# Optimization experiments

Hardware: AMD Instinct MI355X
Metric: run time of the kernel (lower is better)

Reference implementation:

```python
import jax, jax.numpy as jnp
import numpy as np

DIM = 1024
CTX_DIM = 1024
VALUE_DIM = 1024
HEADS = 16
HEAD_DIM = DIM // HEADS        # q/k head dim = 64
V_HEAD_DIM = VALUE_DIM // HEADS
LN_EPS = 1e-5


def setup_inputs() -> dict:
    key = jax.random.key(0)
    k0, k1, k2, k3, k4 = jax.random.split(key, 5)
    B, N, M = 4, 1024, 1024
    x = jax.random.normal(k0, (B, N, DIM), jnp.float32)
    context = jax.random.normal(k1, (B, M, CTX_DIM), jnp.float32)
    # Linear weights stored as [in, out] (y = x @ W), matching torch Linear math
    Wq = jax.random.normal(k2, (DIM, DIM), jnp.float32) * (DIM ** -0.5)
    Wkv = jax.random.normal(k3, (CTX_DIM, DIM + VALUE_DIM), jnp.float32) * (CTX_DIM ** -0.5)
    Wt = jax.random.normal(k4, (HEADS, HEADS), jnp.float32) * (HEADS ** -0.5)
    gamma = jnp.ones((HEADS,), jnp.float32)
    beta = jnp.zeros((HEADS,), jnp.float32)
    return {"x": x, "context": context, "Wq": Wq, "Wkv": Wkv,
            "Wt": Wt, "gamma": gamma, "beta": beta}


def reference(x, context, Wq, Wkv, Wt, gamma, beta):
    B, N, _ = x.shape
    M = context.shape[1]
    # projections
    q = (x @ Wq).reshape(B, N, HEADS, HEAD_DIM).transpose(0, 2, 1, 3)       # [B,H,N,d]
    kv = context @ Wkv                                                      # [B,M,dim+vdim]
    k = kv[..., :DIM].reshape(B, M, HEADS, HEAD_DIM).transpose(0, 2, 1, 3)  # [B,H,M,d]
    v = kv[..., DIM:].reshape(B, M, HEADS, V_HEAD_DIM).transpose(0, 2, 1, 3)
    # scaled dot-product scores, fully materialized as in the original
    scale = HEAD_DIM ** -0.5
    dots = jnp.einsum('bhid,bhjd->bhij', q * scale, k)                      # [B,H,N,M]
    w = jax.nn.softmax(dots, axis=-1)
    # talking heads: Linear(heads,heads,bias=False) then LayerNorm(heads) over head axis
    w = jnp.einsum('bhij,hg->bgij', w, Wt)
    mu = jnp.mean(w, axis=1, keepdims=True)
    var = jnp.var(w, axis=1, keepdims=True)
    w = (w - mu) * jax.lax.rsqrt(var + LN_EPS)
    w = w * gamma[None, :, None, None] + beta[None, :, None, None]
    attn = jnp.einsum('bhij,bhjd->bhid', w, v)                              # [B,H,N,vd]
    out = attn.transpose(0, 2, 1, 3).reshape(B, N, VALUE_DIM)
    return out
```

## Files before the change

### kernel.cpp

```cpp
#include <hip/hip_runtime.h>
#include <hip/hip_bf16.h>

typedef __bf16 bf16;
typedef bf16 bf16x2 __attribute__((ext_vector_type(2)));
typedef bf16 bf16x4 __attribute__((ext_vector_type(4)));
typedef bf16 bf16x8 __attribute__((ext_vector_type(8)));
typedef float floatx4 __attribute__((ext_vector_type(4)));

#define MFMA_BF16(a, b, c) __builtin_amdgcn_mfma_f32_16x16x32_bf16((a), (b), (c), 0, 0, 0)

__global__ __launch_bounds__(256) void cvt_kernel(const float* __restrict__ in,
                                                  bf16* __restrict__ out, int n8) {
    int idx = blockIdx.x * 256 + threadIdx.x;
    if (idx >= n8) return;
    const float* src = in + (size_t)idx * 8;
    float4 f0 = *(const float4*)src;
    float4 f1 = *(const float4*)(src + 4);
    bf16x8 v = {(bf16)f0.x, (bf16)f0.y, (bf16)f0.z, (bf16)f0.w,
                (bf16)f1.x, (bf16)f1.y, (bf16)f1.z, (bf16)f1.w};
    *(bf16x8*)(out + (size_t)idx * 8) = v;
}

__global__ __launch_bounds__(256) void trans_kernel(const float* __restrict__ in,
                                                    bf16* __restrict__ out, int R, int C) {
    __shared__ float tile[32][33];
    const int t = threadIdx.x;
    const int r0 = blockIdx.y * 32, c0 = blockIdx.x * 32;
    int r = t >> 3, c4 = (t & 7) * 4;
    float4 v = *(const float4*)&in[(size_t)(r0 + r) * C + c0 + c4];
    tile[r][c4 + 0] = v.x; tile[r][c4 + 1] = v.y;
    tile[r][c4 + 2] = v.z; tile[r][c4 + 3] = v.w;
    __syncthreads();
    int rp = t >> 3, cp = (t & 7) * 4;
    bf16x4 w = {(bf16)tile[cp + 0][rp], (bf16)tile[cp + 1][rp],
                (bf16)tile[cp + 2][rp], (bf16)tile[cp + 3][rp]};
    *(bf16x4*)&out[(size_t)(c0 + rp) * R + r0 + cp] = w;
}

__global__ __launch_bounds__(256) void vtrans_kernel(const bf16* __restrict__ in,
                                                     bf16* __restrict__ out) {
    __shared__ bf16 tile[32][36];
    const int t = threadIdx.x;
    const int r0 = blockIdx.y * 32, c0 = blockIdx.x * 32;
    int r = t >> 3, c4 = (t & 7) * 4;
    bf16x4 v = *(const bf16x4*)&in[(size_t)(r0 + r) * 1024 + c0 + c4];
    tile[r][c4 + 0] = v[0]; tile[r][c4 + 1] = v[1];
    tile[r][c4 + 2] = v[2]; tile[r][c4 + 3] = v[3];
    __syncthreads();
    int rp = t >> 3, cp = (t & 7) * 4;
    int hd = c0 + rp;
    int b = r0 >> 10, j = (r0 & 1023) + cp;
    bf16x4 w = {tile[cp + 0][rp], tile[cp + 1][rp], tile[cp + 2][rp], tile[cp + 3][rp]};
    *(bf16x4*)&out[(size_t)(b * 1024 + hd) * 1024 + j] = w;
}

__global__ __launch_bounds__(256) void prep_wt_kernel(const float* __restrict__ Wt,
                                                      bf16* __restrict__ WtcT) {
    const int t = threadIdx.x;
    const int g = t >> 4, k = t & 15;
    float s = 0.f;
#pragma unroll
    for (int gg = 0; gg < 16; ++gg) s += Wt[k * 16 + gg];
    WtcT[g * 32 + k] = (bf16)(Wt[k * 16 + g] - s * 0.0625f);
    WtcT[g * 32 + 16 + k] = (bf16)0.f;
}

template <int MODE>
__global__ __launch_bounds__(256) void gemm128(const bf16* __restrict__ A,
                                               const bf16* __restrict__ B,
                                               bf16* __restrict__ C,
                                               bf16* __restrict__ V, int N) {
    __shared__ bf16 As[128 * 40];
    __shared__ bf16 Bs[128 * 40];
    const int t = threadIdx.x;
    const int wv = t >> 6, lane = t & 63, quad = lane >> 4, l15 = lane & 15;
    const int wr = wv >> 1, wc = wv & 1;
    const int m0 = blockIdx.y * 128, n0 = blockIdx.x * 128;
    const int ra = t >> 1, kc = (t & 1) * 16;

    floatx4 acc[4][4] = {};

    for (int k0 = 0; k0 < 1024; k0 += 32) {
        bf16x8 a0 = *(const bf16x8*)&A[(size_t)(m0 + ra) * 1024 + k0 + kc];
        bf16x8 a1 = *(const bf16x8*)&A[(size_t)(m0 + ra) * 1024 + k0 + kc + 8];
        bf16x8 b0 = *(const bf16x8*)&B[(size_t)(n0 + ra) * 1024 + k0 + kc];
        bf16x8 b1 = *(const bf16x8*)&B[(size_t)(n0 + ra) * 1024 + k0 + kc + 8];
        __syncthreads();
        *(bf16x8*)&As[ra * 40 + kc] = a0;
        *(bf16x8*)&As[ra * 40 + kc + 8] = a1;
        *(bf16x8*)&Bs[ra * 40 + kc] = b0;
        *(bf16x8*)&Bs[ra * 40 + kc + 8] = b1;
        __syncthreads();
        bf16x8 af[4], bfr[4];
#pragma unroll
        for (int mt = 0; mt < 4; ++mt)
            af[mt] = *(bf16x8*)&As[(wr * 64 + mt * 16 + l15) * 40 + quad * 8];
#pragma unroll
        for (int nt = 0; nt < 4; ++nt)
            bfr[nt] = *(bf16x8*)&Bs[(wc * 64 + nt * 16 + l15) * 40 + quad * 8];
#pragma unroll
        for (int mt = 0; mt < 4; ++mt)
#pragma unroll
            for (int nt = 0; nt < 4; ++nt)
                acc[mt][nt] = MFMA_BF16(af[mt], bfr[nt], acc[mt][nt]);
    }
#pragma unroll
    for (int mt = 0; mt < 4; ++mt)
#pragma unroll
        for (int nt = 0; nt < 4; ++nt)
#pragma unroll
            for (int r = 0; r < 4; ++r) {
                int m = m0 + wr * 64 + mt * 16 + quad * 4 + r;
                int n = n0 + wc * 64 + nt * 16 + l15;
                bf16 val = (bf16)acc[mt][nt][r];
                if (MODE == 0) {
                    C[(size_t)m * N + n] = val;
                } else {
                    if (n < 1024) C[(size_t)m * 1024 + n] = val;
                    else          V[(size_t)m * 1024 + (n - 1024)] = val;
                }
            }
}

__global__ __launch_bounds__(256, 4) void denom_kernel(const bf16* __restrict__ Qb,
                                                       const bf16* __restrict__ Kb,
                                                       float* __restrict__ L) {
    const int t = threadIdx.x;
    const int wv = t >> 6, lane = t & 63, quad = lane >> 4, l15 = lane & 15;
    unsigned n = blockIdx.x + (blockIdx.y << 5) + (blockIdx.z << 7);
    unsigned o = (n & 7) * 256 + (n >> 3);
    const int i0 = (o & 31) * 32;
    const int b  = (o >> 5) & 3;
    const int jz = o >> 7;
    const float scale = 0.125f;
    const bf16* Kbase = Kb + (size_t)b * 1024 * 1024;

    for (int hh = 0; hh < 4; ++hh) {
        const int h = wv * 4 + hh;
        bf16x8 qa[2][2];
#pragma unroll
        for (int it = 0; it < 2; ++it) {
            const bf16* qp = Qb + (size_t)(b * 1024 + i0 + it * 16 + l15) * 1024 +
                             h * 64 + quad * 8;
            qa[it][0] = *(const bf16x8*)qp;
            qa[it][1] = *(const bf16x8*)(qp + 32);
        }
        floatx4 se[2] = {};
#pragma unroll
        for (int jt = 0; jt < 4; ++jt) {
            int j = jz * 64 + jt * 16 + l15;
            const bf16* kp = Kbase + (size_t)j * 1024 + h * 64 + quad * 8;
            bf16x8 k0 = *(const bf16x8*)kp;
            bf16x8 k1 = *(const bf16x8*)(kp + 32);
#pragma unroll
            for (int it = 0; it < 2; ++it) {
                floatx4 c = {0.f, 0.f, 0.f, 0.f};
                c = MFMA_BF16(qa[it][0], k0, c);
                c = MFMA_BF16(qa[it][1], k1, c);
#pragma unroll
                for (int r = 0; r < 4; ++r) se[it][r] += __expf(c[r] * scale);
            }
        }
#pragma unroll
        for (int it = 0; it < 2; ++it)
#pragma unroll
            for (int r = 0; r < 4; ++r) {
                float s = se[it][r];
                s += __shfl_xor(s, 1); s += __shfl_xor(s, 2);
                s += __shfl_xor(s, 4); s += __shfl_xor(s, 8);
                if (l15 == 0)
                    atomicAdd(&L[(size_t)(b * 16 + h) * 1024 + i0 + it * 16 +
                                 quad * 4 + r], s);
            }
    }
}

__global__ __launch_bounds__(512, 4) void attn_kernel(const bf16* __restrict__ Qb,
                                                      const bf16* __restrict__ Kb,
                                                      const bf16* __restrict__ Vt,
                                                      const float* __restrict__ L,
                                                      const bf16* __restrict__ WtcT,
                                                      const float* __restrict__ gamma,
                                                      const float* __restrict__ beta,
                                                      float* __restrict__ out) {
    __shared__ bf16 Buf1[2][512 * 20];
    __shared__ bf16 Buf2[2][16 * 640];
    const int t = threadIdx.x;
    const int wv = t >> 6, lane = t & 63, quad = lane >> 4, l15 = lane & 15;
    unsigned n = blockIdx.x + (blockIdx.y << 6) + (blockIdx.z << 8);
    unsigned o_idx = (n & 7) * 64 + (n >> 3);
    const int i0 = (o_idx & 63) * 16;
    const int b  = (o_idx >> 6) & 3;
    const int jz = o_idx >> 8;
    const float scale = 0.125f;

    if (t < 8) Buf2[0][2560 + t] = (bf16)0.f;
    const bf16* Zbuf = &Buf2[0][2560];

    bf16x8 a_wt = *(const bf16x8*)&WtcT[l15 * 32 + quad * 8];
    float gq[4], bq[4];
#pragma unroll
    for (int r = 0; r < 4; ++r) { gq[r] = gamma[quad * 4 + r]; bq[r] = beta[quad * 4 + r]; }

    bf16x8 qa[2][2];
    float invl[2][4];
#pragma unroll
    for (int hh = 0; hh < 2; ++hh) {
        int h = wv * 2 + hh;
        const bf16* qp = Qb + (size_t)(b * 1024 + i0 + l15) * 1024 + h * 64 + quad * 8;
        qa[hh][0] = *(const bf16x8*)qp;
        qa[hh][1] = *(const bf16x8*)(qp + 32);
#pragma unroll
        for (int r = 0; r < 4; ++r)
            invl[hh][r] = 1.f / L[(size_t)(b * 16 + h) * 1024 + i0 + quad * 4 + r];
    }

    const bf16* Kbase = Kb + (size_t)b * 1024 * 1024;
    const bf16* Vbase = Vt + (size_t)b * 16 * 64 * 1024;
    floatx4 o[2][4] = {};

    auto S_phase = [&](int jt) {
        bf16* B1 = Buf1[jt & 1];
        const int j0 = jz * 512 + jt * 32;
#pragma unroll
        for (int ns = 0; ns < 2; ++ns) {
            floatx4 cw[2];
#pragma unroll
            for (int hh = 0; hh < 2; ++hh) {
                int h = wv * 2 + hh;
                const bf16* kp = Kbase + (size_t)(j0 + ns * 16 + l15) * 1024 + h * 64 + quad * 8;
                floatx4 c = {0.f, 0.f, 0.f, 0.f};
                c = MFMA_BF16(qa[hh][0], *(const bf16x8*)kp, c);
                c = MFMA_BF16(qa[hh][1], *(const bf16x8*)(kp + 32), c);
                cw[hh] = c;
            }
#pragma unroll
            for (int r = 0; r < 4; ++r) {
                bf16x2 pk = {(bf16)(__expf(cw[0][r] * scale) * invl[0][r]),
                             (bf16)(__expf(cw[1][r] * scale) * invl[1][r])};
                *(bf16x2*)&B1[((quad * 4 + r) * 32 + ns * 16 + l15) * 20 + wv * 2] = pk;
            }
        }
    };
    auto MIX = [&](int jt) {
        const bf16* B1 = Buf1[jt & 1];
        bf16* B2 = Buf2[jt & 1];
#pragma unroll
        for (int grp = 0; grp < 4; ++grp) {
            int gi = wv * 4 + grp, ig = gi >> 1, jb = (gi & 1) * 16;
            int p = ig * 32 + jb + l15;
            const bf16* src = (quad < 2) ? &B1[p * 20 + quad * 8] : Zbuf;
            floatx4 c = {0.f, 0.f, 0.f, 0.f};
            c = MFMA_BF16(a_wt, *(const bf16x8*)src, c);
            float s2 = c[0] * c[0] + c[1] * c[1] + c[2] * c[2] + c[3] * c[3];
            s2 += __shfl_xor(s2, 16);
            s2 += __shfl_xor(s2, 32);
            float rs = rsqrtf(s2 * 0.0625f + 1e-5f);
#pragma unroll
            for (int r = 0; r < 4; ++r) {
                float w2 = c[r] * rs * gq[r] + bq[r];
                B2[(quad * 4 + r) * 640 + (quad & 1) * 8 + ig * 40 + jb + l15] = (bf16)w2;
            }
        }
    };
    auto PV = [&](int jt) {
        const bf16* B2 = Buf2[jt & 1];
        const int j0 = jz * 512 + jt * 32;
#pragma unroll
        for (int hh = 0; hh < 2; ++hh) {
            int g = wv * 2 + hh;
            bf16x8 a = *(const bf16x8*)&B2[g * 640 + ((g >> 2) & 1) * 8 + l15 * 40 + quad * 8];
#pragma unroll
            for (int dt = 0; dt < 4; ++dt) {
                const bf16* vp = Vbase + (size_t)(g * 64 + dt * 16 + l15) * 1024 + j0 + quad * 8;
                o[hh][dt] = MFMA_BF16(a, *(const bf16x8*)vp, o[hh][dt]);
            }
        }
    };

    S_phase(0);
    __syncthreads();
    S_phase(1); MIX(0);
    __syncthreads();
    for (int jt = 2; jt < 16; ++jt) {
        S_phase(jt); PV(jt - 2); MIX(jt - 1);
        __syncthreads();
    }
    PV(14); MIX(15);
    __syncthreads();
    PV(15);

#pragma unroll
    for (int hh = 0; hh < 2; ++hh) {
        int g = wv * 2 + hh;
#pragma unroll
        for (int dt = 0; dt < 4; ++dt)
#pragma unroll
            for (int r = 0; r < 4; ++r)
                atomicAdd(&out[(size_t)(b * 1024 + i0 + quad * 4 + r) * 1024 +
                               g * 64 + dt * 16 + l15], o[hh][dt][r]);
    }
}

extern "C" void kernel_launch(void* const* d_in, const int* in_sizes, int n_in,
                              void* d_out, int out_size, void* d_ws, size_t ws_size,
                              hipStream_t stream) {
    const float* x     = (const float*)d_in[0];
    const float* ctx   = (const float*)d_in[1];
    const float* Wq    = (const float*)d_in[2];
    const float* Wkv   = (const float*)d_in[3];
    const float* Wt    = (const float*)d_in[4];
    const float* gamma = (const float*)d_in[5];
    const float* beta  = (const float*)d_in[6];
    float* out = (float*)d_out;

    bf16* xb   = (bf16*)d_ws;
    bf16* cb   = xb + (size_t)4 * 1024 * 1024;
    bf16* WqT  = cb + (size_t)4 * 1024 * 1024;
    bf16* WkvT = WqT + (size_t)1024 * 1024;
    bf16* Qb   = WkvT + (size_t)2048 * 1024;
    bf16* Kb   = Qb + (size_t)4 * 1024 * 1024;
    bf16* Vr   = Kb + (size_t)4 * 1024 * 1024;
    bf16* Vt   = Vr + (size_t)4 * 1024 * 1024;
    float* L   = (float*)(Vt + (size_t)4 * 1024 * 1024);
    bf16* WtcT = Vr;

    hipMemsetAsync(L, 0, (size_t)4 * 16 * 1024 * sizeof(float), stream);
    hipMemsetAsync(out, 0, (size_t)out_size * sizeof(float), stream);

    cvt_kernel<<<2048, 256, 0, stream>>>(x, xb, 524288);
    cvt_kernel<<<2048, 256, 0, stream>>>(ctx, cb, 524288);
    trans_kernel<<<dim3(32, 32), 256, 0, stream>>>(Wq, WqT, 1024, 1024);
    trans_kernel<<<dim3(64, 32), 256, 0, stream>>>(Wkv, WkvT, 1024, 2048);

    gemm128<0><<<dim3(8, 32), 256, 0, stream>>>(xb, WqT, Qb, nullptr, 1024);
    gemm128<1><<<dim3(16, 32), 256, 0, stream>>>(cb, WkvT, Kb, Vr, 2048);
    vtrans_kernel<<<dim3(32, 128), 256, 0, stream>>>(Vr, Vt);
    prep_wt_kernel<<<1, 256, 0, stream>>>(Wt, WtcT);

    denom_kernel<<<dim3(32, 4, 16), 256, 0, stream>>>(Qb, Kb, L);
    attn_kernel<<<dim3(64, 4, 2), 512, 0, stream>>>(Qb, Kb, Vt, L, WtcT, gamma, beta, out);
}
```

Baseline: 369.5 us.

## Fuse softmax denominator computation into attention kernel, removing denom kernel

```diff
diff --git a/kernel.cpp b/kernel.cpp
--- a/kernel.cpp
+++ b/kernel.cpp
@@ -122,63 +122,9 @@
             }
 }
 
-__global__ __launch_bounds__(256, 4) void denom_kernel(const bf16* __restrict__ Qb,
-                                                       const bf16* __restrict__ Kb,
-                                                       float* __restrict__ L) {
-    const int t = threadIdx.x;
-    const int wv = t >> 6, lane = t & 63, quad = lane >> 4, l15 = lane & 15;
-    unsigned n = blockIdx.x + (blockIdx.y << 5) + (blockIdx.z << 7);
-    unsigned o = (n & 7) * 256 + (n >> 3);
-    const int i0 = (o & 31) * 32;
-    const int b  = (o >> 5) & 3;
-    const int jz = o >> 7;
-    const float scale = 0.125f;
-    const bf16* Kbase = Kb + (size_t)b * 1024 * 1024;
-
-    for (int hh = 0; hh < 4; ++hh) {
-        const int h = wv * 4 + hh;
-        bf16x8 qa[2][2];
-#pragma unroll
-        for (int it = 0; it < 2; ++it) {
-            const bf16* qp = Qb + (size_t)(b * 1024 + i0 + it * 16 + l15) * 1024 +
-                             h * 64 + quad * 8;
-            qa[it][0] = *(const bf16x8*)qp;
-            qa[it][1] = *(const bf16x8*)(qp + 32);
-        }
-        floatx4 se[2] = {};
-#pragma unroll
-        for (int jt = 0; jt < 4; ++jt) {
-            int j = jz * 64 + jt * 16 + l15;
-            const bf16* kp = Kbase + (size_t)j * 1024 + h * 64 + quad * 8;
-            bf16x8 k0 = *(const bf16x8*)kp;
-            bf16x8 k1 = *(const bf16x8*)(kp + 32);
-#pragma unroll
-            for (int it = 0; it < 2; ++it) {
-                floatx4 c = {0.f, 0.f, 0.f, 0.f};
-                c = MFMA_BF16(qa[it][0], k0, c);
-                c = MFMA_BF16(qa[it][1], k1, c);
-#pragma unroll
-                for (int r = 0; r < 4; ++r) se[it][r] += __expf(c[r] * scale);
-            }
-        }
-#pragma unroll
-        for (int it = 0; it < 2; ++it)
-#pragma unroll
-            for (int r = 0; r < 4; ++r) {
-                float s = se[it][r];
-                s += __shfl_xor(s, 1); s += __shfl_xor(s, 2);
-                s += __shfl_xor(s, 4); s += __shfl_xor(s, 8);
-                if (l15 == 0)
-                    atomicAdd(&L[(size_t)(b * 16 + h) * 1024 + i0 + it * 16 +
-                                 quad * 4 + r], s);
-            }
-    }
-}
-
 __global__ __launch_bounds__(512, 4) void attn_kernel(const bf16* __restrict__ Qb,
                                                       const bf16* __restrict__ Kb,
                                                       const bf16* __restrict__ Vt,
-                                                      const float* __restrict__ L,
                                                       const bf16* __restrict__ WtcT,
                                                       const float* __restrict__ gamma,
                                                       const float* __restrict__ beta,
@@ -203,20 +149,45 @@
     for (int r = 0; r < 4; ++r) { gq[r] = gamma[quad * 4 + r]; bq[r] = beta[quad * 4 + r]; }
 
     bf16x8 qa[2][2];
-    float invl[2][4];
 #pragma unroll
     for (int hh = 0; hh < 2; ++hh) {
         int h = wv * 2 + hh;
         const bf16* qp = Qb + (size_t)(b * 1024 + i0 + l15) * 1024 + h * 64 + quad * 8;
         qa[hh][0] = *(const bf16x8*)qp;
         qa[hh][1] = *(const bf16x8*)(qp + 32);
-#pragma unroll
-        for (int r = 0; r < 4; ++r)
-            invl[hh][r] = 1.f / L[(size_t)(b * 16 + h) * 1024 + i0 + quad * 4 + r];
     }
 
     const bf16* Kbase = Kb + (size_t)b * 1024 * 1024;
     const bf16* Vbase = Vt + (size_t)b * 16 * 64 * 1024;
+
+    float invl[2][4];
+    {
+        floatx4 se[2] = {};
+#pragma unroll 2
+        for (int jt = 0; jt < 64; ++jt) {
+            int j = jt * 16 + l15;
+            const bf16* kr = Kbase + (size_t)j * 1024 + quad * 8;
+#pragma unroll
+            for (int hh = 0; hh < 2; ++hh) {
+                const bf16* kp = kr + (wv * 2 + hh) * 64;
+                floatx4 c = {0.f, 0.f, 0.f, 0.f};
+                c = MFMA_BF16(qa[hh][0], *(const bf16x8*)kp, c);
+                c = MFMA_BF16(qa[hh][1], *(const bf16x8*)(kp + 32), c);
+#pragma unroll
+                for (int r = 0; r < 4; ++r) se[hh][r] += __expf(c[r] * scale);
+            }
+        }
+#pragma unroll
+        for (int hh = 0; hh < 2; ++hh)
+#pragma unroll
+            for (int r = 0; r < 4; ++r) {
+                float s = se[hh][r];
+                s += __shfl_xor(s, 1); s += __shfl_xor(s, 2);
+                s += __shfl_xor(s, 4); s += __shfl_xor(s, 8);
+                invl[hh][r] = 1.f / s;
+            }
+    }
+
     floatx4 o[2][4] = {};
 
     auto S_phase = [&](int jt) {
@@ -322,10 +293,8 @@
     bf16* Kb   = Qb + (size_t)4 * 1024 * 1024;
     bf16* Vr   = Kb + (size_t)4 * 1024 * 1024;
     bf16* Vt   = Vr + (size_t)4 * 1024 * 1024;
-    float* L   = (float*)(Vt + (size_t)4 * 1024 * 1024);
     bf16* WtcT = Vr;
 
-    hipMemsetAsync(L, 0, (size_t)4 * 16 * 1024 * sizeof(float), stream);
     hipMemsetAsync(out, 0, (size_t)out_size * sizeof(float), stream);
 
     cvt_kernel<<<2048, 256, 0, stream>>>(x, xb, 524288);
@@ -338,6 +307,5 @@
     vtrans_kernel<<<dim3(32, 128), 256, 0, stream>>>(Vr, Vt);
     prep_wt_kernel<<<1, 256, 0, stream>>>(Wt, WtcT);
 
-    denom_kernel<<<dim3(32, 4, 16), 256, 0, stream>>>(Qb, Kb, L);
-    attn_kernel<<<dim3(64, 4, 2), 512, 0, stream>>>(Qb, Kb, Vt, L, WtcT, gamma, beta, out);
-}
+    attn_kernel<<<dim3(64, 4, 2), 512, 0, stream>>>(Qb, Kb, Vt, WtcT, gamma, beta, out);
+}
```

Measured after the change: 425.2 us. +15.1%, slower.
